# Kernel optimization log

Hardware: AMD Instinct MI355X
Metric: run time of the kernel (lower is better)

## Reference

```python
import jax, jax.numpy as jnp
from jax import lax
import numpy as np


def conv2d(x, w, pad):
    # x: NCHW, w: OIHW
    return lax.conv_general_dilated(
        x, w, window_strides=(1, 1), padding=[(pad, pad), (pad, pad)],
        dimension_numbers=("NCHW", "OIHW", "NCHW"))


def _scan_dir(x, a, axis, reverse):
    """Directional IRNN scan: cur = relu(x_i + alpha * prev), prev0 = 0.
    a broadcasts as (1, C, 1) over the remaining (B, C, L) slice dims."""
    if reverse:
        x = jnp.flip(x, axis)
    xs = jnp.moveaxis(x, axis, 0)  # (L, B, C, other)

    def step(prev, xi):
        cur = jax.nn.relu(xi + a * prev)
        return cur, cur

    _, hs = lax.scan(step, jnp.zeros_like(xs[0]), xs)
    h = jnp.moveaxis(hs, 0, axis)
    if reverse:
        h = jnp.flip(h, axis)
    return h


def spatial_irnn(x, alpha):
    a = alpha.reshape(1, -1, 1)  # broadcasts over (B, C, W) or (B, C, H)
    h_td = _scan_dir(x, a, axis=2, reverse=False)  # top -> down
    h_dt = _scan_dir(x, a, axis=2, reverse=True)   # down -> top
    h_lr = _scan_dir(x, a, axis=3, reverse=False)  # left -> right
    h_rl = _scan_dir(x, a, axis=3, reverse=True)   # right -> left
    return h_td, h_lr, h_dt, h_rl


def setup_inputs() -> dict:
    key = jax.random.key(0)
    ks = jax.random.split(key, 10)
    B, C, H, W = 8, 32, 256, 256
    mid = C // 2
    s = 0.05
    return {
        "x": jax.random.normal(ks[0], (B, C, H, W), jnp.float32),
        "alpha1": jnp.full((C,), 0.2, jnp.float32),
        "alpha2": jnp.full((C,), 0.2, jnp.float32),
        "w_in": jax.random.normal(ks[1], (C, C, 3, 3), jnp.float32) * s,
        "w2": jax.random.normal(ks[2], (C, 4 * C, 3, 3), jnp.float32) * s,
        "w3": jax.random.normal(ks[3], (C, 4 * C, 3, 3), jnp.float32) * s,
        "att_w1": jax.random.normal(ks[4], (mid, C, 3, 3), jnp.float32) * s,
        "att_w2": jax.random.normal(ks[5], (mid, mid, 3, 3), jnp.float32) * s,
        "att_w3": jax.random.normal(ks[6], (4, mid, 1, 1), jnp.float32) * s,
        "att_b3": jnp.zeros((4,), jnp.float32),
        "w_out": jax.random.normal(ks[7], (1, C, 1, 1), jnp.float32) * s,
    }


def reference(x, alpha1, alpha2, w_in, w2, w3, att_w1, att_w2, att_w3, att_b3, w_out):
    # Attention gate: 4 per-direction weight maps in (0,1)
    a = jax.nn.relu(conv2d(x, att_w1, pad=1))
    a = jax.nn.relu(conv2d(a, att_w2, pad=1))
    weight = jax.nn.sigmoid(conv2d(a, att_w3, pad=0) + att_b3.reshape(1, -1, 1, 1))

    def gate(up, right, down, left):
        return jnp.concatenate([
            up * weight[:, 0:1], right * weight[:, 1:2],
            down * weight[:, 2:3], left * weight[:, 3:4]], axis=1)

    out = conv2d(x, w_in, pad=1)
    up, right, down, left = spatial_irnn(out, alpha1)
    out = conv2d(gate(up, right, down, left), w2, pad=1)
    up, right, down, left = spatial_irnn(out, alpha2)
    out = jax.nn.relu(conv2d(gate(up, right, down, left), w3, pad=1))
    mask = jax.nn.sigmoid(conv2d(out, w_out, pad=0))
    return mask
```

## Files before the change

### kernel.cpp

```cpp
#include <hip/hip_runtime.h>
#include <cstddef>

#define H_ 256
#define W_ 256
#define HW_ 65536

typedef unsigned int uint;
typedef unsigned short ushort;
typedef __attribute__((ext_vector_type(8))) short short8;
typedef __attribute__((ext_vector_type(16))) float floatx16;

__device__ __forceinline__ float bf2f(ushort u) {
    return __uint_as_float(((uint)u) << 16);
}
__device__ __forceinline__ ushort f2bf(float f) {
    uint u = __float_as_uint(f);
    uint r = (u + 0x7fffu + ((u >> 16) & 1u)) >> 16;
    return (ushort)r;
}
__device__ __forceinline__ float sigmoidf_(float x) {
    return 1.0f / (1.0f + expf(-x));
}

__device__ __forceinline__ void prep_one(const float* src, ushort* dst,
                                         int CO, int CI, int e) {
    int chunk = e / 9216;
    int r = e - chunk * 9216;
    int co = r / 288;
    int kk = r - co * 288;
    int khw = kk >> 5;
    int ci = kk & 31;
    int cig = chunk * 32 + ci;
    float v = 0.f;
    if (co < CO && cig < CI) v = src[(co * CI + cig) * 9 + khw];
    int s = kk >> 4;
    int lane = ((kk >> 3) & 1) * 32 + co;
    int j = kk & 7;
    dst[(((size_t)chunk * 18 + s) * 64 + lane) * 8 + j] = f2bf(v);
}

__global__ __launch_bounds__(256) void prep_weights(
    const float* __restrict__ w_in, const float* __restrict__ w2,
    const float* __restrict__ w3, const float* __restrict__ aw1,
    const float* __restrict__ aw2,
    ushort* __restrict__ w_inB, ushort* __restrict__ w2B,
    ushort* __restrict__ w3B, ushort* __restrict__ aw1B,
    ushort* __restrict__ aw2B, ushort* __restrict__ zp) {
    int idx = blockIdx.x * 256 + threadIdx.x;
    if (idx < 64) zp[idx] = 0;
    if (idx < 9216)        prep_one(w_in, w_inB, 32, 32, idx);
    else if (idx < 46080)  prep_one(w2, w2B, 32, 128, idx - 9216);
    else if (idx < 82944)  prep_one(w3, w3B, 32, 128, idx - 46080);
    else if (idx < 92160)  prep_one(aw1, aw1B, 16, 32, idx - 82944);
    else if (idx < 101376) prep_one(aw2, aw2B, 16, 16, idx - 92160);
}

__global__ __launch_bounds__(256) void transform_x(const float* __restrict__ x,
                                                   ushort* __restrict__ xh) {
    __shared__ float s[64][33];
    const int t = threadIdx.x;
    const int w0 = blockIdx.x * 64, h = blockIdx.y, b = blockIdx.z;
    {
        int ww = t & 63, c0 = (t >> 6) * 8;
#pragma unroll
        for (int j = 0; j < 8; j++) {
            int c = c0 + j;
            s[ww][c] = x[((size_t)(b * 32 + c)) * HW_ + h * W_ + w0 + ww];
        }
    }
    __syncthreads();
    {
        int p = t >> 2, cb = t & 3;
        ushort tmp[8];
#pragma unroll
        for (int j = 0; j < 8; j++) tmp[j] = f2bf(s[p][cb * 8 + j]);
        *(uint4*)(xh + (((size_t)b * HW_ + h * W_ + w0 + p) * 32) + cb * 8) =
            *(const uint4*)tmp;
    }
}

template<int NCHUNK, int COOUT, bool RELU>
__global__ __launch_bounds__(256, 4) void conv_mfma(
    const ushort* __restrict__ in0, const ushort* __restrict__ in1,
    const ushort* __restrict__ in2, const ushort* __restrict__ in3,
    const ushort* __restrict__ wB, const ushort* __restrict__ zp,
    ushort* __restrict__ outp) {
    __shared__ __align__(16) ushort smem[1360 * 8];
    const int t = threadIdx.x;
    const int wid = t >> 6;
    const int lane = t & 63;
    const int lco = lane & 31, lhalf = lane >> 5;
    const int w0 = blockIdx.x * 32, h0 = blockIdx.y * 8, b = blockIdx.z;
    const ushort* ins[4] = {in0, in1, in2, in3};

    floatx16 acc0, acc1;
#pragma unroll
    for (int i = 0; i < 16; i++) { acc0[i] = 0.f; acc1[i] = 0.f; }

    for (int ch = 0; ch < NCHUNK; ch++) {
        __syncthreads();
        {
            const ushort* inp = ins[ch];
#pragma unroll
            for (int i = 0; i < 6; i++) {
                int u = i * 256 + t;
                if (u < 1360) {
                    int row = u / 136;
                    int rem = u - row * 136;
                    int cb = rem / 34;
                    int p = rem - cb * 34;
                    int gh = h0 - 1 + row, gw = w0 - 1 + p;
                    const ushort* src = ((unsigned)gh < 256u && (unsigned)gw < 256u)
                        ? (inp + (((size_t)b * HW_ + (size_t)gh * W_ + gw) * 32 + cb * 8))
                        : zp;
                    __builtin_amdgcn_global_load_lds(
                        (const __attribute__((address_space(1))) unsigned int*)src,
                        (__attribute__((address_space(3))) unsigned int*)(smem + (size_t)(i * 256 + (t & ~63)) * 8),
                        16, 0, 0);
                }
            }
        }
        __syncthreads();

        const ushort* wbp = wB + ((size_t)ch * 18 * 64 + lane) * 8;
#pragma unroll
        for (int half = 0; half < 2; half++) {
            short8 bf[9];
#pragma unroll
            for (int j = 0; j < 9; j++)
                bf[j] = *(const short8*)(wbp + (size_t)(2 * j + half) * 512);
            const int cbr = half * 2 + lhalf;
#pragma unroll
            for (int kw = 0; kw < 3; kw++) {
                const int ww = lco + kw;
                short8 a[4];
#pragma unroll
                for (int r = 0; r < 4; r++)
                    a[r] = *(const short8*)(smem + (size_t)((wid * 2 + r) * 136 + cbr * 34 + ww) * 8);
#pragma unroll
                for (int kh = 0; kh < 3; kh++) {
                    acc0 = __builtin_amdgcn_mfma_f32_32x32x16_bf16(a[kh], bf[kh * 3 + kw], acc0, 0, 0, 0);
                    acc1 = __builtin_amdgcn_mfma_f32_32x32x16_bf16(a[kh + 1], bf[kh * 3 + kw], acc1, 0, 0, 0);
                }
            }
        }
    }

#pragma unroll
    for (int r = 0; r < 16; r++) {
        int prow = (r & 3) + 8 * (r >> 2) + 4 * lhalf;
        float v0 = acc0[r], v1 = acc1[r];
        if (RELU) { v0 = fmaxf(v0, 0.f); v1 = fmaxf(v1, 0.f); }
        ushort u0 = (lco < COOUT) ? f2bf(v0) : (ushort)0;
        ushort u1 = (lco < COOUT) ? f2bf(v1) : (ushort)0;
        size_t p0 = (((size_t)b * HW_ + (h0 + wid * 2) * W_ + w0 + prow) * 32) + lco;
        outp[p0] = u0;
        outp[p0 + (size_t)W_ * 32] = u1;
    }
}

__global__ __launch_bounds__(256) void att1x1(const ushort* __restrict__ a2,
                                              const float* __restrict__ w,
                                              const float* __restrict__ bias,
                                              ushort* __restrict__ wmapT) {
    int idx = blockIdx.x * 256 + threadIdx.x;
    float xin[16];
    {
        uint4 v0 = *(const uint4*)(a2 + (size_t)idx * 32);
        uint4 v1 = *(const uint4*)(a2 + (size_t)idx * 32 + 8);
        const ushort* u = (const ushort*)&v0;
#pragma unroll
        for (int j = 0; j < 8; j++) xin[j] = bf2f(u[j]);
        const ushort* u2 = (const ushort*)&v1;
#pragma unroll
        for (int j = 0; j < 8; j++) xin[8 + j] = bf2f(u2[j]);
    }
#pragma unroll
    for (int g = 0; g < 4; g++) {
        float acc = bias[g];
#pragma unroll
        for (int ci = 0; ci < 16; ci++) acc = fmaf(xin[ci], w[g * 16 + ci], acc);
        wmapT[(size_t)g * 8 * HW_ + idx] = f2bf(sigmoidf_(acc));
    }
}

__global__ __launch_bounds__(256) void out1x1(const ushort* __restrict__ feat,
                                              const float* __restrict__ w,
                                              float* __restrict__ out) {
    int idx = blockIdx.x * 256 + threadIdx.x;
    float acc = 0.f;
    const ushort* f = feat + (size_t)idx * 32;
#pragma unroll
    for (int q = 0; q < 4; q++) {
        uint4 v = *(const uint4*)(f + q * 8);
        const ushort* u = (const ushort*)&v;
#pragma unroll
        for (int j = 0; j < 8; j++) acc = fmaf(bf2f(u[j]), w[q * 8 + j], acc);
    }
    out[idx] = sigmoidf_(acc);
}

template<int VERT>
__global__ __launch_bounds__(256) void scan_seg(
    const ushort* __restrict__ feat, const float* __restrict__ alpha,
    const ushort* __restrict__ wmapT, ushort* __restrict__ gfwd,
    ushort* __restrict__ gbwd, int gf, int gb) {
    const int t = threadIdx.x;
    const int cg = t & 3;
    const int bx = blockIdx.x;
    const int col = (bx & 3) * 64 + (t >> 2);
    const int seg = (bx >> 2) & 7;
    const int dir = (bx >> 5) & 1;
    const int b = bx >> 6;
    const int c0 = cg * 8;

    float a[8];
#pragma unroll
    for (int j = 0; j < 8; j++) a[j] = alpha[c0 + j];

    const ushort* wplane = wmapT + (size_t)(dir ? gb : gf) * 8 * HW_ + (size_t)b * HW_;
    ushort* gout = dir ? gbwd : gfwd;

    const int main0 = seg * 32;
    const int start = (seg == 0) ? 0 : main0 - 16;
    const int cnt = main0 - start + 32;

    auto pixof = [&](int p) -> size_t {
        int phys = dir ? 255 - p : p;
        return VERT ? ((size_t)phys * W_ + col) : ((size_t)col * W_ + phys);
    };

    uint4 xv[4];
    ushort wv[4];
#pragma unroll
    for (int k = 0; k < 4; k++) {
        size_t pix = pixof(start + k);
        xv[k] = *(const uint4*)(feat + ((size_t)b * HW_ + pix) * 32 + c0);
        wv[k] = wplane[pix];
    }
    float prev[8];
#pragma unroll
    for (int j = 0; j < 8; j++) prev[j] = 0.f;

    for (int i = 0; i < cnt; i += 4) {
#pragma unroll
        for (int k = 0; k < 4; k++) {
            const int p = start + i + k;
            uint4 xcur = xv[k];
            ushort wcur = wv[k];
            if (i + k + 4 < cnt) {
                size_t pix = pixof(p + 4);
                xv[k] = *(const uint4*)(feat + ((size_t)b * HW_ + pix) * 32 + c0);
                wv[k] = wplane[pix];
            }
            const ushort* xu = (const ushort*)&xcur;
            if (p >= main0) {
                float wmv = bf2f(wcur);
                ushort o[8];
#pragma unroll
                for (int j = 0; j < 8; j++) {
                    float cur = fmaxf(fmaf(a[j], prev[j], bf2f(xu[j])), 0.f);
                    prev[j] = cur;
                    o[j] = f2bf(cur * wmv);
                }
                *(uint4*)(gout + ((size_t)b * HW_ + pixof(p)) * 32 + c0) = *(const uint4*)o;
            } else {
#pragma unroll
                for (int j = 0; j < 8; j++)
                    prev[j] = fmaxf(fmaf(a[j], prev[j], bf2f(xu[j])), 0.f);
            }
        }
    }
}

extern "C" void kernel_launch(void* const* d_in, const int* in_sizes, int n_in,
                              void* d_out, int out_size, void* d_ws, size_t ws_size,
                              hipStream_t stream) {
    const float* x      = (const float*)d_in[0];
    const float* alpha1 = (const float*)d_in[1];
    const float* alpha2 = (const float*)d_in[2];
    const float* w_in   = (const float*)d_in[3];
    const float* w2     = (const float*)d_in[4];
    const float* w3     = (const float*)d_in[5];
    const float* aw1    = (const float*)d_in[6];
    const float* aw2    = (const float*)d_in[7];
    const float* aw3    = (const float*)d_in[8];
    const float* ab3    = (const float*)d_in[9];
    const float* wout   = (const float*)d_in[10];
    float* out = (float*)d_out;

    const size_t TEN = (size_t)8 * HW_ * 32;
    ushort* p = (ushort*)d_ws;
    ushort* xh    = p; p += TEN;
    ushort* feat  = p; p += TEN;
    ushort* g0    = p; p += TEN;
    ushort* g1    = p; p += TEN;
    ushort* g2    = p; p += TEN;
    ushort* g3    = p; p += TEN;
    ushort* wmapT = p; p += (size_t)4 * 8 * HW_;
    ushort* w_inB = p; p += 9216;
    ushort* w2B   = p; p += 36864;
    ushort* w3B   = p; p += 36864;
    ushort* aw1B  = p; p += 9216;
    ushort* aw2B  = p; p += 9216;
    ushort* zp    = p; p += 64;

    prep_weights<<<396, 256, 0, stream>>>(w_in, w2, w3, aw1, aw2,
                                          w_inB, w2B, w3B, aw1B, aw2B, zp);
    transform_x<<<dim3(4, 256, 8), 256, 0, stream>>>(x, xh);

    dim3 gconv(8, 32, 8);
    conv_mfma<1, 16, true><<<gconv, 256, 0, stream>>>(xh, xh, xh, xh, aw1B, zp, g0);
    conv_mfma<1, 16, true><<<gconv, 256, 0, stream>>>(g0, g0, g0, g0, aw2B, zp, g1);
    att1x1<<<2048, 256, 0, stream>>>(g1, aw3, ab3, wmapT);

    conv_mfma<1, 32, false><<<gconv, 256, 0, stream>>>(xh, xh, xh, xh, w_inB, zp, feat);

    scan_seg<1><<<512, 256, 0, stream>>>(feat, alpha1, wmapT, g0, g2, 0, 2);
    scan_seg<0><<<512, 256, 0, stream>>>(feat, alpha1, wmapT, g1, g3, 1, 3);

    conv_mfma<4, 32, false><<<gconv, 256, 0, stream>>>(g0, g1, g2, g3, w2B, zp, feat);

    scan_seg<1><<<512, 256, 0, stream>>>(feat, alpha2, wmapT, g0, g2, 0, 2);
    scan_seg<0><<<512, 256, 0, stream>>>(feat, alpha2, wmapT, g1, g3, 1, 3);

    conv_mfma<4, 32, true><<<gconv, 256, 0, stream>>>(g0, g1, g2, g3, w3B, zp, feat);

    out1x1<<<2048, 256, 0, stream>>>(feat, wout, out);
}
```

Before: 399.1 us.

## Replace direct-to-LDS loads with register staging and XOR-swizzled LDS layout

The conv kernel's input tile was loaded with global_load_lds into a channel-block-major LDS layout using a zero page for padding. It now precomputes global offsets and LDS slots once, loads through registers with zero-fill for out-of-bounds pixels, and stores into a pixel-major layout with an XOR swizzle on the channel block. The MFMA operand reads use the matching swizzled index. The swizzle is meant to cut LDS bank conflicts on the A-fragment reads and the zero-page buffer goes away, at the cost of extra registers and losing the asynchronous direct-to-LDS path.

```diff
diff --git a/kernel.cpp b/kernel.cpp
--- a/kernel.cpp
+++ b/kernel.cpp
@@ -45,9 +45,8 @@
     const float* __restrict__ aw2,
     ushort* __restrict__ w_inB, ushort* __restrict__ w2B,
     ushort* __restrict__ w3B, ushort* __restrict__ aw1B,
-    ushort* __restrict__ aw2B, ushort* __restrict__ zp) {
+    ushort* __restrict__ aw2B) {
     int idx = blockIdx.x * 256 + threadIdx.x;
-    if (idx < 64) zp[idx] = 0;
     if (idx < 9216)        prep_one(w_in, w_inB, 32, 32, idx);
     else if (idx < 46080)  prep_one(w2, w2B, 32, 128, idx - 9216);
     else if (idx < 82944)  prep_one(w3, w3B, 32, 128, idx - 46080);
@@ -83,8 +82,7 @@
 __global__ __launch_bounds__(256, 4) void conv_mfma(
     const ushort* __restrict__ in0, const ushort* __restrict__ in1,
     const ushort* __restrict__ in2, const ushort* __restrict__ in3,
-    const ushort* __restrict__ wB, const ushort* __restrict__ zp,
-    ushort* __restrict__ outp) {
+    const ushort* __restrict__ wB, ushort* __restrict__ outp) {
     __shared__ __align__(16) ushort smem[1360 * 8];
     const int t = threadIdx.x;
     const int wid = t >> 6;
@@ -93,6 +91,21 @@
     const int w0 = blockIdx.x * 32, h0 = blockIdx.y * 8, b = blockIdx.z;
     const ushort* ins[4] = {in0, in1, in2, in3};
 
+    size_t goff[6];
+    int slot[6];
+    bool ok[6];
+#pragma unroll
+    for (int i = 0; i < 6; i++) {
+        int u = i * 256 + t;
+        int row = u / 136;
+        int rem = u - row * 136;
+        int p = rem >> 2, cb = rem & 3;
+        int gh = h0 - 1 + row, gw = w0 - 1 + p;
+        ok[i] = (u < 1360) && ((unsigned)gh < 256u) && ((unsigned)gw < 256u);
+        goff[i] = ok[i] ? ((((size_t)b * HW_ + (size_t)gh * W_ + gw) * 32) + cb * 8) : 0;
+        slot[i] = row * 136 + (p << 2) + (cb ^ (p & 3) ^ ((p >> 2) & 3));
+    }
+
     floatx16 acc0, acc1;
 #pragma unroll
     for (int i = 0; i < 16; i++) { acc0[i] = 0.f; acc1[i] = 0.f; }
@@ -101,23 +114,16 @@
         __syncthreads();
         {
             const ushort* inp = ins[ch];
+            uint4 v[6];
+#pragma unroll
+            for (int i = 0; i < 6; i++) {
+                v[i] = make_uint4(0, 0, 0, 0);
+                if (ok[i]) v[i] = *(const uint4*)(inp + goff[i]);
+            }
 #pragma unroll
             for (int i = 0; i < 6; i++) {
                 int u = i * 256 + t;
-                if (u < 1360) {
-                    int row = u / 136;
-                    int rem = u - row * 136;
-                    int cb = rem / 34;
-                    int p = rem - cb * 34;
-                    int gh = h0 - 1 + row, gw = w0 - 1 + p;
-                    const ushort* src = ((unsigned)gh < 256u && (unsigned)gw < 256u)
-                        ? (inp + (((size_t)b * HW_ + (size_t)gh * W_ + gw) * 32 + cb * 8))
-                        : zp;
-                    __builtin_amdgcn_global_load_lds(
-                        (const __attribute__((address_space(1))) unsigned int*)src,
-                        (__attribute__((address_space(3))) unsigned int*)(smem + (size_t)(i * 256 + (t & ~63)) * 8),
-                        16, 0, 0);
-                }
+                if (u < 1360) *(uint4*)(smem + (size_t)slot[i] * 8) = v[i];
             }
         }
         __syncthreads();
@@ -133,10 +139,11 @@
 #pragma unroll
             for (int kw = 0; kw < 3; kw++) {
                 const int ww = lco + kw;
+                const int cbs = cbr ^ (ww & 3) ^ ((ww >> 2) & 3);
                 short8 a[4];
 #pragma unroll
                 for (int r = 0; r < 4; r++)
-                    a[r] = *(const short8*)(smem + (size_t)((wid * 2 + r) * 136 + cbr * 34 + ww) * 8);
+                    a[r] = *(const short8*)(smem + (size_t)((wid * 2 + r) * 136 + (ww << 2) + cbs) * 8);
 #pragma unroll
                 for (int kh = 0; kh < 3; kh++) {
                     acc0 = __builtin_amdgcn_mfma_f32_32x32x16_bf16(a[kh], bf[kh * 3 + kw], acc0, 0, 0, 0);
@@ -303,28 +310,27 @@
     ushort* w3B   = p; p += 36864;
     ushort* aw1B  = p; p += 9216;
     ushort* aw2B  = p; p += 9216;
-    ushort* zp    = p; p += 64;
 
     prep_weights<<<396, 256, 0, stream>>>(w_in, w2, w3, aw1, aw2,
-                                          w_inB, w2B, w3B, aw1B, aw2B, zp);
+                                          w_inB, w2B, w3B, aw1B, aw2B);
     transform_x<<<dim3(4, 256, 8), 256, 0, stream>>>(x, xh);
 
     dim3 gconv(8, 32, 8);
-    conv_mfma<1, 16, true><<<gconv, 256, 0, stream>>>(xh, xh, xh, xh, aw1B, zp, g0);
-    conv_mfma<1, 16, true><<<gconv, 256, 0, stream>>>(g0, g0, g0, g0, aw2B, zp, g1);
+    conv_mfma<1, 16, true><<<gconv, 256, 0, stream>>>(xh, xh, xh, xh, aw1B, g0);
+    conv_mfma<1, 16, true><<<gconv, 256, 0, stream>>>(g0, g0, g0, g0, aw2B, g1);
     att1x1<<<2048, 256, 0, stream>>>(g1, aw3, ab3, wmapT);
 
-    conv_mfma<1, 32, false><<<gconv, 256, 0, stream>>>(xh, xh, xh, xh, w_inB, zp, feat);
+    conv_mfma<1, 32, false><<<gconv, 256, 0, stream>>>(xh, xh, xh, xh, w_inB, feat);
 
     scan_seg<1><<<512, 256, 0, stream>>>(feat, alpha1, wmapT, g0, g2, 0, 2);
     scan_seg<0><<<512, 256, 0, stream>>>(feat, alpha1, wmapT, g1, g3, 1, 3);
 
-    conv_mfma<4, 32, false><<<gconv, 256, 0, stream>>>(g0, g1, g2, g3, w2B, zp, feat);
+    conv_mfma<4, 32, false><<<gconv, 256, 0, stream>>>(g0, g1, g2, g3, w2B, feat);
 
     scan_seg<1><<<512, 256, 0, stream>>>(feat, alpha2, wmapT, g0, g2, 0, 2);
     scan_seg<0><<<512, 256, 0, stream>>>(feat, alpha2, wmapT, g1, g3, 1, 3);
 
-    conv_mfma<4, 32, true><<<gconv, 256, 0, stream>>>(g0, g1, g2, g3, w3B, zp, feat);
+    conv_mfma<4, 32, true><<<gconv, 256, 0, stream>>>(g0, g1, g2, g3, w3B, feat);
 
     out1x1<<<2048, 256, 0, stream>>>(feat, wout, out);
 }
```

Result: no change. 405.2 us (+1.5%).
